# Kernel tuning notes

Hardware: AMD Instinct MI355X
Metric: run time of the kernel (lower is better)

## Reference

```python
import jax, jax.numpy as jnp
import numpy as np

B, T, W, E, H, EMB, NVOCAB, WIN = 256, 200, 200, 768, 256, 32, 201, 8


def setup_inputs() -> dict:
    key = jax.random.key(0)
    ks = jax.random.split(key, 12)
    s = 0.05
    inputs = jax.random.normal(ks[0], (B, T, E), jnp.float32)
    full_word_embeddings = jax.random.normal(ks[1], (B, W, E), jnp.float32)
    lengths = jax.random.randint(ks[2], (B,), T // 2, T + 1)
    fix = jax.random.randint(ks[3], (B, T), 1, NVOCAB)
    fix_seq = jnp.where(jnp.arange(T)[None, :] < lengths[:, None], fix, 0)
    emb_table = (jax.random.normal(ks[4], (NVOCAB, EMB)) * s).at[0].set(0.0)  # padding_idx=0
    W_ih = jax.random.normal(ks[5], (3 * H, E + EMB)) * s  # torch GRU layout, gates r,z,n
    W_hh = jax.random.normal(ks[6], (3 * H, H)) * s
    b_ih = jax.random.normal(ks[7], (3 * H,)) * s
    b_hh = jax.random.normal(ks[8], (3 * H,)) * s
    W_out = jax.random.normal(ks[9], (E, H)) * s  # output_layer: Linear(H, E)
    b_out = jnp.zeros((E,), jnp.float32)
    W_dur = jax.random.normal(ks[10], (1, H)) * s  # duration_layer: Linear(H, 1)
    b_dur = jnp.zeros((1,), jnp.float32)
    return {"inputs": inputs, "fix_seq": fix_seq, "full_word_embeddings": full_word_embeddings,
            "lengths": lengths, "expert_id": 0, "emb_table": emb_table,
            "W_ih": W_ih, "b_ih": b_ih, "W_hh": W_hh, "b_hh": b_hh,
            "W_out": W_out, "b_out": b_out, "W_dur": W_dur, "b_dur": b_dur}


def _gru(x, W_ih, b_ih, W_hh, b_hh, h_dim):
    # x: [B,T,I]. Precompute input projections once, scan over time.
    xg = jnp.einsum('bti,gi->btg', x, W_ih) + b_ih  # [B,T,3H]

    def step(h, xg_t):
        hg = h @ W_hh.T + b_hh
        xr, xz, xn = jnp.split(xg_t, 3, axis=-1)
        hr, hz, hn = jnp.split(hg, 3, axis=-1)
        r = jax.nn.sigmoid(xr + hr)
        z = jax.nn.sigmoid(xz + hz)
        n = jnp.tanh(xn + r * hn)
        h_new = (1.0 - z) * n + z * h
        return h_new, h_new

    h0 = jnp.zeros((x.shape[0], h_dim), x.dtype)
    _, outs = jax.lax.scan(step, h0, jnp.swapaxes(xg, 0, 1))
    return jnp.swapaxes(outs, 0, 1)  # [B,T,H]


def reference(inputs, fix_seq, full_word_embeddings, lengths, expert_id,
              emb_table, W_ih, b_ih, W_hh, b_hh, W_out, b_out, W_dur, b_dur):
    del expert_id  # weights of the selected expert are passed directly
    valid_mask = fix_seq != 0
    scan_emb = emb_table[fix_seq]  # [B,T,32]
    rnn_in = jnp.concatenate([inputs, scan_emb], axis=-1)
    outputs = _gru(rnn_in, W_ih, b_ih, W_hh, b_hh, W_hh.shape[1])  # [B,T,H]
    # pad_packed_sequence zeros outputs beyond each sequence length
    tmask = jnp.arange(outputs.shape[1])[None, :] < lengths[:, None]
    outputs = outputs * tmask[..., None].astype(outputs.dtype)
    # dot attention: proj then scores against word embeddings
    proj = outputs @ W_out.T + b_out  # [B,T,E]
    logits = jnp.einsum('bte,bwe->btw', proj, full_word_embeddings)
    # saccade window mask around current fixation position
    wpos = jnp.arange(full_word_embeddings.shape[1])[None, None, :]
    dist = jnp.abs(wpos - fix_seq[..., None])
    sacc = (dist <= WIN) & valid_mask[..., None]
    logits = jnp.where(sacc, logits, -1e9)
    word_mask = jnp.sum(jnp.abs(full_word_embeddings), axis=-1) != 0
    logits = jnp.where(word_mask[:, None, :], logits, -1e9)
    dur_pred = (outputs @ W_dur.T + b_dur)[..., 0]  # [B,T]
    return logits, dur_pred
```

## Files before the change

### kernel.cpp

```cpp
#include <hip/hip_runtime.h>
#include <hip/hip_bf16.h>

typedef __attribute__((ext_vector_type(8))) short bf16x8;
typedef __attribute__((ext_vector_type(4))) float f32x4;
typedef __attribute__((ext_vector_type(4))) int   i32x4;

#define NB 256
#define NT 200
#define NW 200
#define NE 768
#define NH 256
#define NEMB 32
#define KIN 800
#define G3H 768
#define MROWS 51200

__device__ __forceinline__ float bf2f(unsigned short h) {
    return __uint_as_float(((unsigned)h) << 16);
}
__device__ __forceinline__ unsigned short f2bf(float f) {
    unsigned u = __float_as_uint(f);
    u += 0x7fff + ((u >> 16) & 1);
    return (unsigned short)(u >> 16);
}
__device__ __forceinline__ float sigm(float x) { return 1.0f / (1.0f + __expf(-x)); }
__device__ __forceinline__ float tanh_fast(float x) {
    float e = __expf(2.0f * x);
    return 1.0f - 2.0f / (e + 1.0f);
}

#if __has_builtin(__builtin_amdgcn_sdot4)
__device__ __forceinline__ int SDOT4(int a, int b, int c) {
    return __builtin_amdgcn_sdot4(a, b, c, false);
}
#else
__device__ __forceinline__ int SDOT4(int a, int b, int c) {
    #pragma unroll
    for (int j = 0; j < 4; j++)
        c += (int)(signed char)(a >> (8 * j)) * (int)(signed char)(b >> (8 * j));
    return c;
}
#endif

__device__ __forceinline__ void gload16(const void* g, void* l) {
    __builtin_amdgcn_global_load_lds((const __attribute__((address_space(1))) unsigned int*)g,
                                     (__attribute__((address_space(3))) unsigned int*)l,
                                     16, 0, 0);
}

__global__ void prep1(const float* __restrict__ inputs, const int* __restrict__ fix_seq,
                      const float* __restrict__ emb, const float* __restrict__ Wih,
                      const float* __restrict__ Wout, const float* __restrict__ bih,
                      const float* __restrict__ bhh,
                      unsigned short* __restrict__ Abf, unsigned short* __restrict__ Wihbf,
                      unsigned short* __restrict__ WoutTbf, float* __restrict__ biasC) {
    const long gid0 = (long)blockIdx.x * blockDim.x + threadIdx.x;
    if (gid0 < G3H) biasC[gid0] = bih[gid0] + (gid0 < 512 ? bhh[gid0] : 0.0f);
    const long NA = (long)MROWS << 7;
    const long NWU = 768L << 7;
    const long NOU = 256L << 7;
    const long total = NA + NWU + NOU;
    for (long u = gid0; u < total; u += (long)gridDim.x * blockDim.x) {
        bf16x8 v;
        unsigned short* dst;
        if (u < NA) {
            const long row = u >> 7;
            const int c = (int)(u & 127);
            if (c >= 100) continue;
            const int c8 = c << 3;
            const float* s;
            if (c8 < NE) {
                s = inputs + row * NE + c8;
            } else {
                int fx = fix_seq[row];
                s = emb + (long)fx * NEMB + (c8 - NE);
            }
            #pragma unroll
            for (int j = 0; j < 8; j++) v[j] = (short)f2bf(s[j]);
            dst = Abf + row * KIN + c8;
        } else if (u < NA + NWU) {
            const long u2 = u - NA;
            const long row = u2 >> 7;
            const int c = (int)(u2 & 127);
            if (c >= 100) continue;
            const int c8 = c << 3;
            const float* s = Wih + row * KIN + c8;
            #pragma unroll
            for (int j = 0; j < 8; j++) v[j] = (short)f2bf(s[j]);
            dst = Wihbf + row * KIN + c8;
        } else {
            const long u3 = u - NA - NWU;
            const long row = u3 >> 7;
            const int c = (int)(u3 & 127);
            if (c >= 96) continue;
            const int c8 = c << 3;
            #pragma unroll
            for (int j = 0; j < 8; j++)
                v[j] = (short)f2bf(Wout[(long)(c8 + j) * NH + row]);
            dst = WoutTbf + row * NE + c8;
        }
        *(bf16x8*)dst = v;
    }
}

__global__ __launch_bounds__(512, 4)
void gemm_bt128(const unsigned short* __restrict__ A,
                const unsigned short* __restrict__ Bw,
                const float* __restrict__ bias,
                unsigned short* __restrict__ Out,
                int M, int N, int K) {
    __shared__ unsigned short As[2][128 * 32];
    __shared__ unsigned short Bs[2][256 * 32];
    const int bid = (int)((blockIdx.x & 7) * (gridDim.x >> 3) + (blockIdx.x >> 3));
    const int nblk = N >> 8;
    const int m0 = (bid / nblk) << 7;
    const int n0 = (bid % nblk) << 8;
    const int tid = threadIdx.x;
    const int lane = tid & 63;
    const int wave = tid >> 6;
    const int wm = (wave >> 2) << 6;
    const int wn = (wave & 3) << 6;
    const int nk = K >> 5;

    const int srow = tid >> 2;
    const int sseg = (tid & 3) << 4;
    const char* gA  = (const char*)(A + (long)(m0 + srow) * K) + sseg;
    const char* gB0 = (const char*)(Bw + (long)(n0 + srow) * K) + sseg;
    const char* gB1 = (const char*)(Bw + (long)(n0 + 128 + srow) * K) + sseg;
    const int lofs = wave * 1024;

    f32x4 acc[4][4] = {};

    gload16(gA,  (char*)As[0] + lofs);
    gload16(gB0, (char*)Bs[0] + lofs);
    gload16(gB1, (char*)Bs[0] + 8192 + lofs);

    int cur = 0;
    for (int kt = 0; kt < nk; kt++) {
        if (kt + 1 < nk) {
            gload16(gA  + (kt + 1) * 64, (char*)As[cur ^ 1] + lofs);
            gload16(gB0 + (kt + 1) * 64, (char*)Bs[cur ^ 1] + lofs);
            gload16(gB1 + (kt + 1) * 64, (char*)Bs[cur ^ 1] + 8192 + lofs);
            asm volatile("s_waitcnt vmcnt(3)" ::: "memory");
        } else {
            asm volatile("s_waitcnt vmcnt(0)" ::: "memory");
        }
        __builtin_amdgcn_sched_barrier(0);
        __builtin_amdgcn_s_barrier();
        __builtin_amdgcn_sched_barrier(0);
        bf16x8 af[4], bfr[4];
        #pragma unroll
        for (int mi = 0; mi < 4; mi++)
            af[mi] = *(const bf16x8*)((const char*)As[cur] +
                        (wm + mi * 16 + (lane & 15)) * 64 + ((lane >> 4) << 4));
        #pragma unroll
        for (int ni = 0; ni < 4; ni++)
            bfr[ni] = *(const bf16x8*)((const char*)Bs[cur] +
                        (wn + ni * 16 + (lane & 15)) * 64 + ((lane >> 4) << 4));
        #pragma unroll
        for (int mi = 0; mi < 4; mi++)
            #pragma unroll
            for (int ni = 0; ni < 4; ni++)
                acc[mi][ni] = __builtin_amdgcn_mfma_f32_16x16x32_bf16(
                                  af[mi], bfr[ni], acc[mi][ni], 0, 0, 0);
        asm volatile("s_waitcnt lgkmcnt(0)" ::: "memory");
        __builtin_amdgcn_sched_barrier(0);
        __builtin_amdgcn_s_barrier();
        __builtin_amdgcn_sched_barrier(0);
        cur ^= 1;
    }
    #pragma unroll
    for (int ni = 0; ni < 4; ni++) {
        const int col = n0 + wn + ni * 16 + (lane & 15);
        const float bv = bias[col];
        #pragma unroll
        for (int mi = 0; mi < 4; mi++) {
            const int row = m0 + wm + mi * 16 + ((lane >> 4) << 2);
            #pragma unroll
            for (int r = 0; r < 4; r++)
                Out[(long)(row + r) * N + col] = f2bf(acc[mi][ni][r] + bv);
        }
    }
}

__global__ __launch_bounds__(512)
void gemmG_f32(const float* __restrict__ fwe,
               const unsigned short* __restrict__ BwT,
               const float* __restrict__ bout,
               unsigned short* __restrict__ G,
               unsigned char* __restrict__ wmask,
               float* __restrict__ dvec) {
    __shared__ unsigned short As[128 * 32];
    __shared__ unsigned short Bs[256 * 32];
    __shared__ float Bo[G3H];
    const int m0 = (int)blockIdx.x << 7;
    const int tid = threadIdx.x;
    const int lane = tid & 63;
    const int wave = tid >> 6;
    const int wm = (wave >> 2) << 6;
    const int wn = (wave & 3) << 6;

    const int arow = tid >> 2;
    const int akq = tid & 3;
    const float* aptr = fwe + (long)(m0 + arow) * NE + akq * 8;
    char* la = (char*)As + arow * 64 + akq * 16;

    const int sseg = (tid & 3) << 4;
    const char* gBa = (const char*)(BwT + (long)arow * NE) + sseg;
    const char* gBb = (const char*)(BwT + (long)(128 + arow) * NE) + sseg;
    char* lBa = (char*)Bs + wave * 1024;
    char* lBb = (char*)Bs + 8192 + wave * 1024;

    for (int i = tid; i < G3H; i += 512) Bo[i] = bout[i];

    float4 fa0 = *(const float4*)(aptr);
    float4 fa1 = *(const float4*)(aptr + 4);

    f32x4 acc[4][4] = {};
    float asum = 0.0f, vdot = 0.0f;

    __syncthreads();

    for (int kt = 0; kt < 24; kt++) {
        __syncthreads();
        gload16(gBa + kt * 64, lBa);
        gload16(gBb + kt * 64, lBb);
        const float* bo = Bo + kt * 32 + akq * 8;
        const float4 b0 = *(const float4*)(bo);
        const float4 b1 = *(const float4*)(bo + 4);
        asum += fabsf(fa0.x) + fabsf(fa0.y) + fabsf(fa0.z) + fabsf(fa0.w)
              + fabsf(fa1.x) + fabsf(fa1.y) + fabsf(fa1.z) + fabsf(fa1.w);
        vdot += fa0.x * b0.x + fa0.y * b0.y + fa0.z * b0.z + fa0.w * b0.w
              + fa1.x * b1.x + fa1.y * b1.y + fa1.z * b1.z + fa1.w * b1.w;
        bf16x8 v;
        v[0] = (short)f2bf(fa0.x); v[1] = (short)f2bf(fa0.y);
        v[2] = (short)f2bf(fa0.z); v[3] = (short)f2bf(fa0.w);
        v[4] = (short)f2bf(fa1.x); v[5] = (short)f2bf(fa1.y);
        v[6] = (short)f2bf(fa1.z); v[7] = (short)f2bf(fa1.w);
        *(bf16x8*)la = v;
        asm volatile("s_waitcnt vmcnt(0)" ::: "memory");
        __syncthreads();
        if (kt + 1 < 24) {
            const float* ap = aptr + (kt + 1) * 32;
            fa0 = *(const float4*)(ap);
            fa1 = *(const float4*)(ap + 4);
        }
        bf16x8 af[4], bfr[4];
        #pragma unroll
        for (int mi = 0; mi < 4; mi++)
            af[mi] = *(const bf16x8*)((const char*)As +
                        (wm + mi * 16 + (lane & 15)) * 64 + ((lane >> 4) << 4));
        #pragma unroll
        for (int ni = 0; ni < 4; ni++)
            bfr[ni] = *(const bf16x8*)((const char*)Bs +
                        (wn + ni * 16 + (lane & 15)) * 64 + ((lane >> 4) << 4));
        #pragma unroll
        for (int mi = 0; mi < 4; mi++)
            #pragma unroll
            for (int ni = 0; ni < 4; ni++)
                acc[mi][ni] = __builtin_amdgcn_mfma_f32_16x16x32_bf16(
                                  af[mi], bfr[ni], acc[mi][ni], 0, 0, 0);
    }
    asum += __shfl_xor(asum, 1);  asum += __shfl_xor(asum, 2);
    vdot += __shfl_xor(vdot, 1);  vdot += __shfl_xor(vdot, 2);
    if (akq == 0) {
        wmask[m0 + arow] = (asum != 0.0f) ? 1 : 0;
        dvec[m0 + arow] = vdot;
    }
    #pragma unroll
    for (int ni = 0; ni < 4; ni++) {
        const int col = wn + ni * 16 + (lane & 15);
        #pragma unroll
        for (int mi = 0; mi < 4; mi++) {
            const int row = m0 + wm + mi * 16 + ((lane >> 4) << 2);
            #pragma unroll
            for (int r = 0; r < 4; r++)
                G[(long)(row + r) * NH + col] = f2bf(acc[mi][ni][r]);
        }
    }
}

__global__ __launch_bounds__(512, 2)
__attribute__((amdgpu_waves_per_eu(2, 2)))
void gru_scan(const unsigned short* __restrict__ xg,
              const float* __restrict__ Whh,
              const float* __restrict__ bhh,
              const int* __restrict__ lengths,
              unsigned short* __restrict__ hout) {
    __shared__ __align__(16) unsigned char h8[2][256];
    const int tid = threadIdx.x;
    const int lane = tid & 63;
    const int wave = tid >> 6;
    const int b = blockIdx.x;
    const int col = wave * 32 + (lane & 31);
    const int kh = lane >> 5;

    int W[3][32];
    #pragma unroll
    for (int g = 0; g < 3; g++) {
        const float* wr = Whh + (long)(g * 256 + col) * NH + kh * 128;
        #pragma unroll
        for (int d = 0; d < 32; d++) {
            const float4 f = *(const float4*)(wr + d * 4);
            unsigned pack = 0;
            #pragma unroll
            for (int j = 0; j < 4; j++) {
                const float fv = j == 0 ? f.x : j == 1 ? f.y : j == 2 ? f.z : f.w;
                int wq = (int)rintf(fv * 400.0f);
                wq = wq > 127 ? 127 : (wq < -127 ? -127 : wq);
                pack |= ((unsigned)(wq & 0xff)) << (8 * j);
            }
            W[g][d] = (int)pack;
        }
    }
    const float bhn = bhh[512 + col];
    const int len = lengths[b];
    if (tid < 128) ((unsigned*)h8)[tid] = 0u;

    const unsigned short* xrow = xg + (long)b * NT * G3H;
    unsigned short xv0 = xrow[col], xv1 = xrow[256 + col], xv2 = xrow[512 + col];
    float hp = 0.0f;
    const float ISC = 1.0f / (400.0f * 127.0f);
    const bool wlo = (lane < 32);

    asm volatile("s_waitcnt lgkmcnt(0)" ::: "memory");
    __builtin_amdgcn_sched_barrier(0);
    __builtin_amdgcn_s_barrier();
    __builtin_amdgcn_sched_barrier(0);

    for (int t = 0; t < NT; t++) {
        const unsigned char* hb = h8[(t + 1) & 1] + kh * 128;
        int p0a = 0, p0b = 0, p1a = 0, p1b = 0, p2a = 0, p2b = 0;
        #pragma unroll
        for (int r = 0; r < 8; r++) {
            const i32x4 hv = *(const i32x4*)(hb + r * 16);
            p0a = SDOT4(hv[0], W[0][r * 4 + 0], p0a);
            p1a = SDOT4(hv[0], W[1][r * 4 + 0], p1a);
            p2a = SDOT4(hv[0], W[2][r * 4 + 0], p2a);
            p0b = SDOT4(hv[1], W[0][r * 4 + 1], p0b);
            p1b = SDOT4(hv[1], W[1][r * 4 + 1], p1b);
            p2b = SDOT4(hv[1], W[2][r * 4 + 1], p2b);
            p0a = SDOT4(hv[2], W[0][r * 4 + 2], p0a);
            p1a = SDOT4(hv[2], W[1][r * 4 + 2], p1a);
            p2a = SDOT4(hv[2], W[2][r * 4 + 2], p2a);
            p0b = SDOT4(hv[3], W[0][r * 4 + 3], p0b);
            p1b = SDOT4(hv[3], W[1][r * 4 + 3], p1b);
            p2b = SDOT4(hv[3], W[2][r * 4 + 3], p2b);
        }
        int p0 = p0a + p0b, p1 = p1a + p1b, p2 = p2a + p2b;
        p0 += __shfl_xor(p0, 32);
        p1 += __shfl_xor(p1, 32);
        p2 += __shfl_xor(p2, 32);
        const float r = sigm(bf2f(xv0) + (float)p0 * ISC);
        const float z = sigm(bf2f(xv1) + (float)p1 * ISC);
        const float n = tanh_fast(bf2f(xv2) + r * ((float)p2 * ISC + bhn));
        hp = (1.0f - z) * n + z * hp;
        if (wlo) {
            h8[t & 1][col] = (unsigned char)((int)rintf(hp * 127.0f) & 0xff);
            hout[((long)b * NT + t) * NH + col] = (t < len) ? f2bf(hp) : (unsigned short)0;
        }
        if (t + 1 < NT) {
            const unsigned short* xn = xrow + (long)(t + 1) * G3H;
            xv0 = xn[col]; xv1 = xn[256 + col]; xv2 = xn[512 + col];
        }
        asm volatile("s_waitcnt lgkmcnt(0)" ::: "memory");
        __builtin_amdgcn_sched_barrier(0);
        __builtin_amdgcn_s_barrier();
        __builtin_amdgcn_sched_barrier(0);
    }
}

__global__ __launch_bounds__(256)
void logits_dur(const unsigned short* __restrict__ Hrow,
                const unsigned short* __restrict__ G,
                const int* __restrict__ fix_seq,
                const unsigned char* __restrict__ wmask,
                const float* __restrict__ dvec,
                const float* __restrict__ Wdur, const float* __restrict__ bdur,
                float* __restrict__ out) {
    __shared__ float dots[4][20];
    const int wv = threadIdx.x >> 6;
    const int gwave = (int)blockIdx.x * 4 + wv;
    const int lane = threadIdx.x & 63;
    const int l16 = lane & 15;
    const int grp = lane >> 4;
    const int b = gwave / NT;

    const unsigned short* hp = Hrow + (long)gwave * NH + l16 * 16;
    const bf16x8 h0 = *(const bf16x8*)hp;
    const bf16x8 h1 = *(const bf16x8*)(hp + 8);
    float hf[16];
    #pragma unroll
    for (int j = 0; j < 8; j++) { hf[j] = bf2f((unsigned short)h0[j]);
                                  hf[8 + j] = bf2f((unsigned short)h1[j]); }

    const int fix = fix_seq[gwave];
    const int wbase = fix - 8;

    if (fix != 0) {
        #pragma unroll
        for (int it = 0; it < 5; it++) {
            const int wi = it * 4 + grp;
            int w = wbase + wi;
            w = w < 0 ? 0 : (w > NW - 1 ? NW - 1 : w);
            const unsigned short* gp = G + ((long)b * NW + w) * NH + l16 * 16;
            const bf16x8 g0 = *(const bf16x8*)gp;
            const bf16x8 g1 = *(const bf16x8*)(gp + 8);
            float p = 0.0f;
            #pragma unroll
            for (int j = 0; j < 8; j++) {
                p += hf[j] * bf2f((unsigned short)g0[j]);
                p += hf[8 + j] * bf2f((unsigned short)g1[j]);
            }
            p += __shfl_xor(p, 1); p += __shfl_xor(p, 2);
            p += __shfl_xor(p, 4); p += __shfl_xor(p, 8);
            if (l16 == 0 && wi < 17) dots[wv][wi] = p;
        }
    }
    float pd = 0.0f;
    #pragma unroll
    for (int j = 0; j < 16; j++) pd += hf[j] * Wdur[l16 * 16 + j];
    pd += __shfl_xor(pd, 1); pd += __shfl_xor(pd, 2);
    pd += __shfl_xor(pd, 4); pd += __shfl_xor(pd, 8);
    if (lane == 0) out[(long)NB * NT * NW + gwave] = pd + bdur[0];

    __syncthreads();

    if (lane < 50) {
        float4 o;
        #pragma unroll
        for (int c = 0; c < 4; c++) {
            const int w = lane * 4 + c;
            const int wi = w - wbase;
            const int wic = wi < 0 ? 0 : (wi > 16 ? 16 : wi);
            const bool ok = (fix != 0) && ((unsigned)wi < 17u) && (wmask[b * NW + w] != 0);
            const float val = dots[wv][wic] + dvec[b * NW + w];
            ((float*)&o)[c] = ok ? val : -1e9f;
        }
        *(float4*)(out + (long)gwave * NW + lane * 4) = o;
    }
}

extern "C" void kernel_launch(void* const* d_in, const int* in_sizes, int n_in,
                              void* d_out, int out_size, void* d_ws, size_t ws_size,
                              hipStream_t stream) {
    (void)in_sizes; (void)n_in; (void)out_size; (void)ws_size;
    const float* inputs  = (const float*)d_in[0];
    const int*   fix_seq = (const int*)d_in[1];
    const float* fwe     = (const float*)d_in[2];
    const int*   lengths = (const int*)d_in[3];
    const float* emb     = (const float*)d_in[5];
    const float* Wih     = (const float*)d_in[6];
    const float* bih     = (const float*)d_in[7];
    const float* Whh     = (const float*)d_in[8];
    const float* bhh     = (const float*)d_in[9];
    const float* Wout    = (const float*)d_in[10];
    const float* bout    = (const float*)d_in[11];
    const float* Wdur    = (const float*)d_in[12];
    const float* bdur    = (const float*)d_in[13];
    float* out = (float*)d_out;

    char* ws = (char*)d_ws;
    unsigned short* Abf     = (unsigned short*)(ws);
    unsigned short* xgbf    = (unsigned short*)(ws + 81920000);
    unsigned short* hout    = (unsigned short*)(ws + 160563200);
    unsigned short* Wihbf   = (unsigned short*)(ws + 186777600);
    unsigned short* WoutTbf = (unsigned short*)(ws + 188006400);
    unsigned char*  wmask   = (unsigned char*)(ws + 188399616);
    float*          biasC   = (float*)(ws + 188450816);
    float*          dvec    = (float*)(ws + 188453888);
    unsigned short* Gbf     = Abf;

    prep1<<<2048, 256, 0, stream>>>(inputs, fix_seq, emb, Wih, Wout, bih, bhh,
                                    Abf, Wihbf, WoutTbf, biasC);
    gemm_bt128<<<400 * 3, 512, 0, stream>>>(Abf, Wihbf, biasC, xgbf, MROWS, G3H, KIN);
    gemmG_f32<<<400, 512, 0, stream>>>(fwe, WoutTbf, bout, Gbf, wmask, dvec);
    gru_scan<<<256, 512, 0, stream>>>(xgbf, Whh, bhh, lengths, hout);
    logits_dur<<<12800, 256, 0, stream>>>(hout, Gbf, fix_seq, wmask, dvec, Wdur, bdur, out);
}
```

Baseline: 461.3 us.

## Fuse input bf16 conversion into X-projection GEMM and use int8 MFMA in GRU scan

The separate pass that converted inputs and the embedding gather to a bf16 staging buffer is removed. The X-projection GEMM now reads fp32 inputs and embeddings directly and converts them in registers, which avoids writing and re-reading roughly 80MB. The GEMM drops double buffering in favour of a single buffer guarded by syncthreads, so load/compute overlap may suffer. The GRU recurrence switches from per-lane SDOT4 loops to int8 16x16x64 MFMA with 1024-thread blocks, but only 16 lanes per wave use the results.

```diff
diff --git a/kernel.cpp b/kernel.cpp
--- a/kernel.cpp
+++ b/kernel.cpp
@@ -29,67 +29,35 @@
     return 1.0f - 2.0f / (e + 1.0f);
 }
 
-#if __has_builtin(__builtin_amdgcn_sdot4)
-__device__ __forceinline__ int SDOT4(int a, int b, int c) {
-    return __builtin_amdgcn_sdot4(a, b, c, false);
-}
-#else
-__device__ __forceinline__ int SDOT4(int a, int b, int c) {
-    #pragma unroll
-    for (int j = 0; j < 4; j++)
-        c += (int)(signed char)(a >> (8 * j)) * (int)(signed char)(b >> (8 * j));
-    return c;
-}
-#endif
-
 __device__ __forceinline__ void gload16(const void* g, void* l) {
     __builtin_amdgcn_global_load_lds((const __attribute__((address_space(1))) unsigned int*)g,
                                      (__attribute__((address_space(3))) unsigned int*)l,
                                      16, 0, 0);
 }
 
-__global__ void prep1(const float* __restrict__ inputs, const int* __restrict__ fix_seq,
-                      const float* __restrict__ emb, const float* __restrict__ Wih,
-                      const float* __restrict__ Wout, const float* __restrict__ bih,
-                      const float* __restrict__ bhh,
-                      unsigned short* __restrict__ Abf, unsigned short* __restrict__ Wihbf,
+__global__ void prep1(const float* __restrict__ Wih, const float* __restrict__ Wout,
+                      const float* __restrict__ bih, const float* __restrict__ bhh,
+                      unsigned short* __restrict__ Wihbf,
                       unsigned short* __restrict__ WoutTbf, float* __restrict__ biasC) {
     const long gid0 = (long)blockIdx.x * blockDim.x + threadIdx.x;
     if (gid0 < G3H) biasC[gid0] = bih[gid0] + (gid0 < 512 ? bhh[gid0] : 0.0f);
-    const long NA = (long)MROWS << 7;
     const long NWU = 768L << 7;
     const long NOU = 256L << 7;
-    const long total = NA + NWU + NOU;
+    const long total = NWU + NOU;
     for (long u = gid0; u < total; u += (long)gridDim.x * blockDim.x) {
         bf16x8 v;
         unsigned short* dst;
-        if (u < NA) {
+        if (u < NWU) {
             const long row = u >> 7;
             const int c = (int)(u & 127);
             if (c >= 100) continue;
             const int c8 = c << 3;
-            const float* s;
-            if (c8 < NE) {
-                s = inputs + row * NE + c8;
-            } else {
-                int fx = fix_seq[row];
-                s = emb + (long)fx * NEMB + (c8 - NE);
-            }
-            #pragma unroll
-            for (int j = 0; j < 8; j++) v[j] = (short)f2bf(s[j]);
-            dst = Abf + row * KIN + c8;
-        } else if (u < NA + NWU) {
-            const long u2 = u - NA;
-            const long row = u2 >> 7;
-            const int c = (int)(u2 & 127);
-            if (c >= 100) continue;
-            const int c8 = c << 3;
             const float* s = Wih + row * KIN + c8;
             #pragma unroll
             for (int j = 0; j < 8; j++) v[j] = (short)f2bf(s[j]);
             dst = Wihbf + row * KIN + c8;
         } else {
-            const long u3 = u - NA - NWU;
+            const long u3 = u - NWU;
             const long row = u3 >> 7;
             const int c = (int)(u3 & 127);
             if (c >= 96) continue;
@@ -103,59 +71,67 @@
     }
 }
 
-__global__ __launch_bounds__(512, 4)
-void gemm_bt128(const unsigned short* __restrict__ A,
-                const unsigned short* __restrict__ Bw,
-                const float* __restrict__ bias,
-                unsigned short* __restrict__ Out,
-                int M, int N, int K) {
-    __shared__ unsigned short As[2][128 * 32];
-    __shared__ unsigned short Bs[2][256 * 32];
+__global__ __launch_bounds__(512)
+void gemmX_f32(const float* __restrict__ inputs,
+               const int* __restrict__ fix_seq,
+               const float* __restrict__ emb,
+               const unsigned short* __restrict__ Bw,
+               const float* __restrict__ bias,
+               unsigned short* __restrict__ Out) {
+    __shared__ unsigned short As[128 * 32];
+    __shared__ unsigned short Bs[256 * 32];
     const int bid = (int)((blockIdx.x & 7) * (gridDim.x >> 3) + (blockIdx.x >> 3));
-    const int nblk = N >> 8;
-    const int m0 = (bid / nblk) << 7;
-    const int n0 = (bid % nblk) << 8;
+    const int m0 = (bid / 3) << 7;
+    const int n0 = (bid % 3) << 8;
     const int tid = threadIdx.x;
     const int lane = tid & 63;
     const int wave = tid >> 6;
     const int wm = (wave >> 2) << 6;
     const int wn = (wave & 3) << 6;
-    const int nk = K >> 5;
-
-    const int srow = tid >> 2;
+
+    const int arow = tid >> 2;
+    const int akq = tid & 3;
+    const float* aptr = inputs + (long)(m0 + arow) * NE + akq * 8;
+    const int fix = fix_seq[m0 + arow];
+    const float* eptr = emb + (long)fix * NEMB + akq * 8;
+    char* la = (char*)As + arow * 64 + akq * 16;
+
     const int sseg = (tid & 3) << 4;
-    const char* gA  = (const char*)(A + (long)(m0 + srow) * K) + sseg;
-    const char* gB0 = (const char*)(Bw + (long)(n0 + srow) * K) + sseg;
-    const char* gB1 = (const char*)(Bw + (long)(n0 + 128 + srow) * K) + sseg;
-    const int lofs = wave * 1024;
+    const char* gBa = (const char*)(Bw + (long)(n0 + arow) * KIN) + sseg;
+    const char* gBb = (const char*)(Bw + (long)(n0 + 128 + arow) * KIN) + sseg;
+    char* lBa = (char*)Bs + wave * 1024;
+    char* lBb = (char*)Bs + 8192 + wave * 1024;
+
+    float4 fa0 = *(const float4*)(aptr);
+    float4 fa1 = *(const float4*)(aptr + 4);
 
     f32x4 acc[4][4] = {};
 
-    gload16(gA,  (char*)As[0] + lofs);
-    gload16(gB0, (char*)Bs[0] + lofs);
-    gload16(gB1, (char*)Bs[0] + 8192 + lofs);
-
-    int cur = 0;
-    for (int kt = 0; kt < nk; kt++) {
-        if (kt + 1 < nk) {
-            gload16(gA  + (kt + 1) * 64, (char*)As[cur ^ 1] + lofs);
-            gload16(gB0 + (kt + 1) * 64, (char*)Bs[cur ^ 1] + lofs);
-            gload16(gB1 + (kt + 1) * 64, (char*)Bs[cur ^ 1] + 8192 + lofs);
-            asm volatile("s_waitcnt vmcnt(3)" ::: "memory");
-        } else {
-            asm volatile("s_waitcnt vmcnt(0)" ::: "memory");
-        }
-        __builtin_amdgcn_sched_barrier(0);
-        __builtin_amdgcn_s_barrier();
-        __builtin_amdgcn_sched_barrier(0);
+    for (int kt = 0; kt < 25; kt++) {
+        __syncthreads();
+        gload16(gBa + kt * 64, lBa);
+        gload16(gBb + kt * 64, lBb);
+        bf16x8 v;
+        v[0] = (short)f2bf(fa0.x); v[1] = (short)f2bf(fa0.y);
+        v[2] = (short)f2bf(fa0.z); v[3] = (short)f2bf(fa0.w);
+        v[4] = (short)f2bf(fa1.x); v[5] = (short)f2bf(fa1.y);
+        v[6] = (short)f2bf(fa1.z); v[7] = (short)f2bf(fa1.w);
+        *(bf16x8*)la = v;
+        asm volatile("s_waitcnt vmcnt(0)" ::: "memory");
+        __syncthreads();
+        if (kt + 1 < 25) {
+            const float* ap = (kt + 1 < 24) ? (aptr + (kt + 1) * 32) : eptr;
+            fa0 = *(const float4*)(ap);
+            fa1 = *(const float4*)(ap + 4);
+        }
         bf16x8 af[4], bfr[4];
         #pragma unroll
         for (int mi = 0; mi < 4; mi++)
-            af[mi] = *(const bf16x8*)((const char*)As[cur] +
+            af[mi] = *(const bf16x8*)((const char*)As +
                         (wm + mi * 16 + (lane & 15)) * 64 + ((lane >> 4) << 4));
         #pragma unroll
         for (int ni = 0; ni < 4; ni++)
-            bfr[ni] = *(const bf16x8*)((const char*)Bs[cur] +
+            bfr[ni] = *(const bf16x8*)((const char*)Bs +
                         (wn + ni * 16 + (lane & 15)) * 64 + ((lane >> 4) << 4));
         #pragma unroll
         for (int mi = 0; mi < 4; mi++)
@@ -163,11 +139,6 @@
             for (int ni = 0; ni < 4; ni++)
                 acc[mi][ni] = __builtin_amdgcn_mfma_f32_16x16x32_bf16(
                                   af[mi], bfr[ni], acc[mi][ni], 0, 0, 0);
-        asm volatile("s_waitcnt lgkmcnt(0)" ::: "memory");
-        __builtin_amdgcn_sched_barrier(0);
-        __builtin_amdgcn_s_barrier();
-        __builtin_amdgcn_sched_barrier(0);
-        cur ^= 1;
     }
     #pragma unroll
     for (int ni = 0; ni < 4; ni++) {
@@ -178,7 +149,7 @@
             const int row = m0 + wm + mi * 16 + ((lane >> 4) << 2);
             #pragma unroll
             for (int r = 0; r < 4; r++)
-                Out[(long)(row + r) * N + col] = f2bf(acc[mi][ni][r] + bv);
+                Out[(long)(row + r) * G3H + col] = f2bf(acc[mi][ni][r] + bv);
         }
     }
 }
@@ -280,8 +251,8 @@
     }
 }
 
-__global__ __launch_bounds__(512, 2)
-__attribute__((amdgpu_waves_per_eu(2, 2)))
+__global__ __launch_bounds__(1024)
+__attribute__((amdgpu_waves_per_eu(4, 4)))
 void gru_scan(const unsigned short* __restrict__ xg,
               const float* __restrict__ Whh,
               const float* __restrict__ bhh,
@@ -292,36 +263,42 @@
     const int lane = tid & 63;
     const int wave = tid >> 6;
     const int b = blockIdx.x;
-    const int col = wave * 32 + (lane & 31);
-    const int kh = lane >> 5;
-
-    int W[3][32];
+    const int l = lane & 15;
+    const int sub = lane >> 4;
+    const int c = wave * 16 + l;
+
+    i32x4 wf[3][4];
     #pragma unroll
     for (int g = 0; g < 3; g++) {
-        const float* wr = Whh + (long)(g * 256 + col) * NH + kh * 128;
-        #pragma unroll
-        for (int d = 0; d < 32; d++) {
-            const float4 f = *(const float4*)(wr + d * 4);
-            unsigned pack = 0;
-            #pragma unroll
-            for (int j = 0; j < 4; j++) {
-                const float fv = j == 0 ? f.x : j == 1 ? f.y : j == 2 ? f.z : f.w;
-                int wq = (int)rintf(fv * 400.0f);
-                wq = wq > 127 ? 127 : (wq < -127 ? -127 : wq);
-                pack |= ((unsigned)(wq & 0xff)) << (8 * j);
+        const float* wr = Whh + (long)(g * 256 + c) * NH;
+        #pragma unroll
+        for (int kt = 0; kt < 4; kt++) {
+            const float* s = wr + kt * 64 + sub * 16;
+            i32x4 v;
+            #pragma unroll
+            for (int q = 0; q < 4; q++) {
+                unsigned pack = 0;
+                #pragma unroll
+                for (int j = 0; j < 4; j++) {
+                    int wq = (int)rintf(s[q * 4 + j] * 400.0f);
+                    wq = wq > 127 ? 127 : (wq < -127 ? -127 : wq);
+                    pack |= ((unsigned)(wq & 0xff)) << (8 * j);
+                }
+                v[q] = (int)pack;
             }
-            W[g][d] = (int)pack;
-        }
-    }
-    const float bhn = bhh[512 + col];
+            wf[g][kt] = v;
+        }
+    }
+    const float bhn = bhh[512 + c];
     const int len = lengths[b];
     if (tid < 128) ((unsigned*)h8)[tid] = 0u;
 
     const unsigned short* xrow = xg + (long)b * NT * G3H;
-    unsigned short xv0 = xrow[col], xv1 = xrow[256 + col], xv2 = xrow[512 + col];
+    const bool gl = (lane < 16);
+    unsigned short xv0 = 0, xv1 = 0, xv2 = 0;
+    if (gl) { xv0 = xrow[c]; xv1 = xrow[256 + c]; xv2 = xrow[512 + c]; }
     float hp = 0.0f;
     const float ISC = 1.0f / (400.0f * 127.0f);
-    const bool wlo = (lane < 32);
 
     asm volatile("s_waitcnt lgkmcnt(0)" ::: "memory");
     __builtin_amdgcn_sched_barrier(0);
@@ -329,39 +306,26 @@
     __builtin_amdgcn_sched_barrier(0);
 
     for (int t = 0; t < NT; t++) {
-        const unsigned char* hb = h8[(t + 1) & 1] + kh * 128;
-        int p0a = 0, p0b = 0, p1a = 0, p1b = 0, p2a = 0, p2b = 0;
-        #pragma unroll
-        for (int r = 0; r < 8; r++) {
-            const i32x4 hv = *(const i32x4*)(hb + r * 16);
-            p0a = SDOT4(hv[0], W[0][r * 4 + 0], p0a);
-            p1a = SDOT4(hv[0], W[1][r * 4 + 0], p1a);
-            p2a = SDOT4(hv[0], W[2][r * 4 + 0], p2a);
-            p0b = SDOT4(hv[1], W[0][r * 4 + 1], p0b);
-            p1b = SDOT4(hv[1], W[1][r * 4 + 1], p1b);
-            p2b = SDOT4(hv[1], W[2][r * 4 + 1], p2b);
-            p0a = SDOT4(hv[2], W[0][r * 4 + 2], p0a);
-            p1a = SDOT4(hv[2], W[1][r * 4 + 2], p1a);
-            p2a = SDOT4(hv[2], W[2][r * 4 + 2], p2a);
-            p0b = SDOT4(hv[3], W[0][r * 4 + 3], p0b);
-            p1b = SDOT4(hv[3], W[1][r * 4 + 3], p1b);
-            p2b = SDOT4(hv[3], W[2][r * 4 + 3], p2b);
-        }
-        int p0 = p0a + p0b, p1 = p1a + p1b, p2 = p2a + p2b;
-        p0 += __shfl_xor(p0, 32);
-        p1 += __shfl_xor(p1, 32);
-        p2 += __shfl_xor(p2, 32);
-        const float r = sigm(bf2f(xv0) + (float)p0 * ISC);
-        const float z = sigm(bf2f(xv1) + (float)p1 * ISC);
-        const float n = tanh_fast(bf2f(xv2) + r * ((float)p2 * ISC + bhn));
-        hp = (1.0f - z) * n + z * hp;
-        if (wlo) {
-            h8[t & 1][col] = (unsigned char)((int)rintf(hp * 127.0f) & 0xff);
-            hout[((long)b * NT + t) * NH + col] = (t < len) ? f2bf(hp) : (unsigned short)0;
-        }
-        if (t + 1 < NT) {
-            const unsigned short* xn = xrow + (long)(t + 1) * G3H;
-            xv0 = xn[col]; xv1 = xn[256 + col]; xv2 = xn[512 + col];
+        const unsigned char* hb = h8[(t + 1) & 1];
+        i32x4 a0 = {}, a1 = {}, a2 = {};
+        #pragma unroll
+        for (int kt = 0; kt < 4; kt++) {
+            const i32x4 af = *(const i32x4*)(hb + kt * 64 + (sub << 4));
+            a0 = __builtin_amdgcn_mfma_i32_16x16x64_i8(af, wf[0][kt], a0, 0, 0, 0);
+            a1 = __builtin_amdgcn_mfma_i32_16x16x64_i8(af, wf[1][kt], a1, 0, 0, 0);
+            a2 = __builtin_amdgcn_mfma_i32_16x16x64_i8(af, wf[2][kt], a2, 0, 0, 0);
+        }
+        if (gl) {
+            const float r = sigm(bf2f(xv0) + (float)a0[0] * ISC);
+            const float z = sigm(bf2f(xv1) + (float)a1[0] * ISC);
+            const float n = tanh_fast(bf2f(xv2) + r * ((float)a2[0] * ISC + bhn));
+            hp = (1.0f - z) * n + z * hp;
+            h8[t & 1][c] = (unsigned char)((int)rintf(hp * 127.0f) & 0xff);
+            hout[((long)b * NT + t) * NH + c] = (t < len) ? f2bf(hp) : (unsigned short)0;
+            if (t + 1 < NT) {
+                const unsigned short* xn = xrow + (long)(t + 1) * G3H;
+                xv0 = xn[c]; xv1 = xn[256 + c]; xv2 = xn[512 + c];
+            }
         }
         asm volatile("s_waitcnt lgkmcnt(0)" ::: "memory");
         __builtin_amdgcn_sched_barrier(0);
@@ -461,7 +425,7 @@
     float* out = (float*)d_out;
 
     char* ws = (char*)d_ws;
-    unsigned short* Abf     = (unsigned short*)(ws);
+    unsigned short* Gbf     = (unsigned short*)(ws);
     unsigned short* xgbf    = (unsigned short*)(ws + 81920000);
     unsigned short* hout    = (unsigned short*)(ws + 160563200);
     unsigned short* Wihbf   = (unsigned short*)(ws + 186777600);
@@ -469,12 +433,10 @@
     unsigned char*  wmask   = (unsigned char*)(ws + 188399616);
     float*          biasC   = (float*)(ws + 188450816);
     float*          dvec    = (float*)(ws + 188453888);
-    unsigned short* Gbf     = Abf;
-
-    prep1<<<2048, 256, 0, stream>>>(inputs, fix_seq, emb, Wih, Wout, bih, bhh,
-                                    Abf, Wihbf, WoutTbf, biasC);
-    gemm_bt128<<<400 * 3, 512, 0, stream>>>(Abf, Wihbf, biasC, xgbf, MROWS, G3H, KIN);
+
+    prep1<<<512, 256, 0, stream>>>(Wih, Wout, bih, bhh, Wihbf, WoutTbf, biasC);
+    gemmX_f32<<<400 * 3, 512, 0, stream>>>(inputs, fix_seq, emb, Wihbf, biasC, xgbf);
     gemmG_f32<<<400, 512, 0, stream>>>(fwe, WoutTbf, bout, Gbf, wmask, dvec);
-    gru_scan<<<256, 512, 0, stream>>>(xgbf, Whh, bhh, lengths, hout);
+    gru_scan<<<256, 1024, 0, stream>>>(xgbf, Whh, bhh, lengths, hout);
     logits_dur<<<12800, 256, 0, stream>>>(hout, Gbf, fix_seq, wmask, dvec, Wdur, bdur, out);
 }
```

Measured after the change: 505.4 us. 1.1x slower.

## Use int8 MFMA for GRU recurrent matvec with 16-column waves

Applied to the files above, without the earlier changes.

Replaces the per-lane sdot4 recurrent matrix-vector product in the GRU scan with int8 MFMA 16x16x64 instructions. Each wave now covers 16 hidden columns, and blocks grow to 1024 threads (16 waves). The h vector is broadcast as the A operand, so only row 0 of each MFMA result is used. Most of the matrix unit's work is wasted, but the per-step serial dot-product chain gets much shorter. Only 16 lanes per wave run the gate math, and the larger block makes the per-step barrier more expensive.

```diff
diff --git a/kernel.cpp b/kernel.cpp
--- a/kernel.cpp
+++ b/kernel.cpp
@@ -28,19 +28,6 @@
     float e = __expf(2.0f * x);
     return 1.0f - 2.0f / (e + 1.0f);
 }
-
-#if __has_builtin(__builtin_amdgcn_sdot4)
-__device__ __forceinline__ int SDOT4(int a, int b, int c) {
-    return __builtin_amdgcn_sdot4(a, b, c, false);
-}
-#else
-__device__ __forceinline__ int SDOT4(int a, int b, int c) {
-    #pragma unroll
-    for (int j = 0; j < 4; j++)
-        c += (int)(signed char)(a >> (8 * j)) * (int)(signed char)(b >> (8 * j));
-    return c;
-}
-#endif
 
 __device__ __forceinline__ void gload16(const void* g, void* l) {
     __builtin_amdgcn_global_load_lds((const __attribute__((address_space(1))) unsigned int*)g,
@@ -280,8 +267,8 @@
     }
 }
 
-__global__ __launch_bounds__(512, 2)
-__attribute__((amdgpu_waves_per_eu(2, 2)))
+__global__ __launch_bounds__(1024)
+__attribute__((amdgpu_waves_per_eu(4, 4)))
 void gru_scan(const unsigned short* __restrict__ xg,
               const float* __restrict__ Whh,
               const float* __restrict__ bhh,
@@ -292,36 +279,42 @@
     const int lane = tid & 63;
     const int wave = tid >> 6;
     const int b = blockIdx.x;
-    const int col = wave * 32 + (lane & 31);
-    const int kh = lane >> 5;
-
-    int W[3][32];
+    const int l = lane & 15;
+    const int sub = lane >> 4;
+    const int c = wave * 16 + l;
+
+    i32x4 wf[3][4];
     #pragma unroll
     for (int g = 0; g < 3; g++) {
-        const float* wr = Whh + (long)(g * 256 + col) * NH + kh * 128;
-        #pragma unroll
-        for (int d = 0; d < 32; d++) {
-            const float4 f = *(const float4*)(wr + d * 4);
-            unsigned pack = 0;
-            #pragma unroll
-            for (int j = 0; j < 4; j++) {
-                const float fv = j == 0 ? f.x : j == 1 ? f.y : j == 2 ? f.z : f.w;
-                int wq = (int)rintf(fv * 400.0f);
-                wq = wq > 127 ? 127 : (wq < -127 ? -127 : wq);
-                pack |= ((unsigned)(wq & 0xff)) << (8 * j);
+        const float* wr = Whh + (long)(g * 256 + c) * NH;
+        #pragma unroll
+        for (int kt = 0; kt < 4; kt++) {
+            const float* s = wr + kt * 64 + sub * 16;
+            i32x4 v;
+            #pragma unroll
+            for (int q = 0; q < 4; q++) {
+                unsigned pack = 0;
+                #pragma unroll
+                for (int j = 0; j < 4; j++) {
+                    int wq = (int)rintf(s[q * 4 + j] * 400.0f);
+                    wq = wq > 127 ? 127 : (wq < -127 ? -127 : wq);
+                    pack |= ((unsigned)(wq & 0xff)) << (8 * j);
+                }
+                v[q] = (int)pack;
             }
-            W[g][d] = (int)pack;
-        }
-    }
-    const float bhn = bhh[512 + col];
+            wf[g][kt] = v;
+        }
+    }
+    const float bhn = bhh[512 + c];
     const int len = lengths[b];
     if (tid < 128) ((unsigned*)h8)[tid] = 0u;
 
     const unsigned short* xrow = xg + (long)b * NT * G3H;
-    unsigned short xv0 = xrow[col], xv1 = xrow[256 + col], xv2 = xrow[512 + col];
+    const bool gl = (lane < 16);
+    unsigned short xv0 = 0, xv1 = 0, xv2 = 0;
+    if (gl) { xv0 = xrow[c]; xv1 = xrow[256 + c]; xv2 = xrow[512 + c]; }
     float hp = 0.0f;
     const float ISC = 1.0f / (400.0f * 127.0f);
-    const bool wlo = (lane < 32);
 
     asm volatile("s_waitcnt lgkmcnt(0)" ::: "memory");
     __builtin_amdgcn_sched_barrier(0);
@@ -329,39 +322,26 @@
     __builtin_amdgcn_sched_barrier(0);
 
     for (int t = 0; t < NT; t++) {
-        const unsigned char* hb = h8[(t + 1) & 1] + kh * 128;
-        int p0a = 0, p0b = 0, p1a = 0, p1b = 0, p2a = 0, p2b = 0;
-        #pragma unroll
-        for (int r = 0; r < 8; r++) {
-            const i32x4 hv = *(const i32x4*)(hb + r * 16);
-            p0a = SDOT4(hv[0], W[0][r * 4 + 0], p0a);
-            p1a = SDOT4(hv[0], W[1][r * 4 + 0], p1a);
-            p2a = SDOT4(hv[0], W[2][r * 4 + 0], p2a);
-            p0b = SDOT4(hv[1], W[0][r * 4 + 1], p0b);
-            p1b = SDOT4(hv[1], W[1][r * 4 + 1], p1b);
-            p2b = SDOT4(hv[1], W[2][r * 4 + 1], p2b);
-            p0a = SDOT4(hv[2], W[0][r * 4 + 2], p0a);
-            p1a = SDOT4(hv[2], W[1][r * 4 + 2], p1a);
-            p2a = SDOT4(hv[2], W[2][r * 4 + 2], p2a);
-            p0b = SDOT4(hv[3], W[0][r * 4 + 3], p0b);
-            p1b = SDOT4(hv[3], W[1][r * 4 + 3], p1b);
-            p2b = SDOT4(hv[3], W[2][r * 4 + 3], p2b);
-        }
-        int p0 = p0a + p0b, p1 = p1a + p1b, p2 = p2a + p2b;
-        p0 += __shfl_xor(p0, 32);
-        p1 += __shfl_xor(p1, 32);
-        p2 += __shfl_xor(p2, 32);
-        const float r = sigm(bf2f(xv0) + (float)p0 * ISC);
-        const float z = sigm(bf2f(xv1) + (float)p1 * ISC);
-        const float n = tanh_fast(bf2f(xv2) + r * ((float)p2 * ISC + bhn));
-        hp = (1.0f - z) * n + z * hp;
-        if (wlo) {
-            h8[t & 1][col] = (unsigned char)((int)rintf(hp * 127.0f) & 0xff);
-            hout[((long)b * NT + t) * NH + col] = (t < len) ? f2bf(hp) : (unsigned short)0;
-        }
-        if (t + 1 < NT) {
-            const unsigned short* xn = xrow + (long)(t + 1) * G3H;
-            xv0 = xn[col]; xv1 = xn[256 + col]; xv2 = xn[512 + col];
+        const unsigned char* hb = h8[(t + 1) & 1];
+        i32x4 a0 = {}, a1 = {}, a2 = {};
+        #pragma unroll
+        for (int kt = 0; kt < 4; kt++) {
+            const i32x4 af = *(const i32x4*)(hb + kt * 64 + (sub << 4));
+            a0 = __builtin_amdgcn_mfma_i32_16x16x64_i8(af, wf[0][kt], a0, 0, 0, 0);
+            a1 = __builtin_amdgcn_mfma_i32_16x16x64_i8(af, wf[1][kt], a1, 0, 0, 0);
+            a2 = __builtin_amdgcn_mfma_i32_16x16x64_i8(af, wf[2][kt], a2, 0, 0, 0);
+        }
+        if (gl) {
+            const float r = sigm(bf2f(xv0) + (float)a0[0] * ISC);
+            const float z = sigm(bf2f(xv1) + (float)a1[0] * ISC);
+            const float n = tanh_fast(bf2f(xv2) + r * ((float)a2[0] * ISC + bhn));
+            hp = (1.0f - z) * n + z * hp;
+            h8[t & 1][c] = (unsigned char)((int)rintf(hp * 127.0f) & 0xff);
+            hout[((long)b * NT + t) * NH + c] = (t < len) ? f2bf(hp) : (unsigned short)0;
+            if (t + 1 < NT) {
+                const unsigned short* xn = xrow + (long)(t + 1) * G3H;
+                xv0 = xn[c]; xv1 = xn[256 + c]; xv2 = xn[512 + c];
+            }
         }
         asm volatile("s_waitcnt lgkmcnt(0)" ::: "memory");
         __builtin_amdgcn_sched_barrier(0);
@@ -475,6 +455,6 @@
                                     Abf, Wihbf, WoutTbf, biasC);
     gemm_bt128<<<400 * 3, 512, 0, stream>>>(Abf, Wihbf, biasC, xgbf, MROWS, G3H, KIN);
     gemmG_f32<<<400, 512, 0, stream>>>(fwe, WoutTbf, bout, Gbf, wmask, dvec);
-    gru_scan<<<256, 512, 0, stream>>>(xgbf, Whh, bhh, lengths, hout);
+    gru_scan<<<256, 1024, 0, stream>>>(xgbf, Whh, bhh, lengths, hout);
     logits_dur<<<12800, 256, 0, stream>>>(hout, Gbf, fix_seq, wmask, dvec, Wdur, bdur, out);
 }
```

After: 452.3 us. Within noise of the previous version (-1.9%).
